# Kernel optimization log

Hardware: AMD Instinct MI355X
Metric: run time of the kernel (lower is better)

## Reference

```python
import jax, jax.numpy as jnp
import numpy as np

B, C, H, W, HEADS = 4, 192, 128, 128, 8
C2 = 2 * C
DN = ('NCHW', 'OIHW', 'NCHW')


def conv1x1(x, w, b):
    o = jax.lax.conv_general_dilated(x, w, (1, 1), 'VALID', dimension_numbers=DN)
    return o + b[None, :, None, None]


def gconv3(x, w, b):
    # grouped 3x3 conv: groups = C, channels = 2C -> 2 in / 2 out channels per group
    o = jax.lax.conv_general_dilated(x, w, (1, 1), 'SAME', dimension_numbers=DN,
                                     feature_group_count=C)
    return o + b[None, :, None, None]


def l2norm(t):
    # torch F.normalize(dim=-1, eps=1e-12)
    n = jnp.linalg.norm(t, axis=-1, keepdims=True)
    return t / jnp.maximum(n, 1e-12)


def setup_inputs() -> dict:
    key = jax.random.key(0)
    ks = jax.random.split(key, 16)
    s = 0.02
    inp = {
        'x': jax.random.normal(ks[0], (B, C, H, W), jnp.float32),
        'y': jax.random.normal(ks[1], (B, C, H, W), jnp.float32),
        'kv_w': jax.random.normal(ks[2], (C2, C, 1, 1), jnp.float32) * s,
        'kv_b': jax.random.normal(ks[3], (C2,), jnp.float32) * s,
        'kv_dw_w': jax.random.normal(ks[4], (C2, 2, 3, 3), jnp.float32) * s,
        'kv_dw_b': jax.random.normal(ks[5], (C2,), jnp.float32) * s,
        'q_w': jax.random.normal(ks[6], (C2, C, 1, 1), jnp.float32) * s,
        'q_b': jax.random.normal(ks[7], (C2,), jnp.float32) * s,
        'q_dw_w': jax.random.normal(ks[8], (C2, 2, 3, 3), jnp.float32) * s,
        'q_dw_b': jax.random.normal(ks[9], (C2,), jnp.float32) * s,
        'ky_w': jax.random.normal(ks[10], (C2, C, 1, 1), jnp.float32) * s,
        'ky_b': jax.random.normal(ks[11], (C2,), jnp.float32) * s,
        'ky_dw_w': jax.random.normal(ks[12], (C2, 2, 3, 3), jnp.float32) * s,
        'ky_dw_b': jax.random.normal(ks[13], (C2,), jnp.float32) * s,
        'temperature': jnp.ones((HEADS, 1, 1), jnp.float32),
        'gamma1': jnp.full((1,), 0.1, jnp.float32),
        'gamma2': jnp.full((1,), 0.1, jnp.float32),
    }
    return inp


def reference(x, y, kv_w, kv_b, kv_dw_w, kv_dw_b, q_w, q_b, q_dw_w, q_dw_b,
              ky_w, ky_b, ky_dw_w, ky_dw_b, temperature, gamma1, gamma2):
    b, c, h, w = x.shape
    ch = c // HEADS  # channels per head

    x_mid = x + y
    q = gconv3(conv1x1(x_mid, kv_w, kv_b), kv_dw_w, kv_dw_b)
    q1, q2 = jnp.split(q, 2, axis=1)
    kvx = gconv3(conv1x1(x, q_w, q_b), q_dw_w, q_dw_b)
    kx, vx = jnp.split(kvx, 2, axis=1)
    kvy = gconv3(conv1x1(y, ky_w, ky_b), ky_dw_w, ky_dw_b)
    ky_, vy = jnp.split(kvy, 2, axis=1)

    def to_heads(t):  # (b, head*ch, h, w) -> (b, head, ch, h*w)
        return t.reshape(b, HEADS, ch, h * w)

    q1, q2, kx, ky_, vx, vy = map(to_heads, (q1, q2, kx, ky_, vx, vy))
    q1, q2, kx, ky_ = map(l2norm, (q1, q2, kx, ky_))

    attn = (jnp.einsum('bhcn,bhdn->bhcd', q1, ky_) +
            jnp.einsum('bhcn,bhdn->bhcd', q2, kx)) * temperature[None]
    attn = jax.nn.softmax(attn, axis=-1)  # (b, head, c, c), tiny c

    out1 = jnp.einsum('bhcd,bhdn->bhcn', attn, vx)
    out2 = jnp.einsum('bhcd,bhdn->bhcn', attn, vy)
    out = gamma1[0] * out1 + gamma2[0] * out2
    return out.reshape(b, c, h, w)
```

## Files before the change

kernel.cpp:

```cpp
#include <hip/hip_runtime.h>
#include <hip/hip_bf16.h>
#include <stdint.h>

#define NUM_B 4
#define NUM_C 192
#define NUM_C2 384
#define NUM_H 128
#define NUM_W 128
#define NUM_N 16384
#define NHEADS 8
#define CHD 24

#define NKC 128
#define PSTRIDE 1280

typedef float f32x4_t __attribute__((ext_vector_type(4)));
typedef float f32x2_t __attribute__((ext_vector_type(2)));
typedef __bf16 bf16x8_t __attribute__((ext_vector_type(8)));
typedef unsigned short u16x8_t __attribute__((ext_vector_type(8)));

__device__ __forceinline__ float bf2f(unsigned short u){
  union { unsigned int i; float f; } v; v.i = ((unsigned int)u) << 16; return v.f;
}
__device__ __forceinline__ unsigned short f2bf(float f){
  union { float f; unsigned int i; } v; v.f = f;
  unsigned int x = v.i;
  x += 0x7fffu + ((x >> 16) & 1u);
  return (unsigned short)(x >> 16);
}
__device__ __forceinline__ unsigned short f2bf_n(float f){
  union { __bf16 h; unsigned short u; } cv; cv.h = (__bf16)f; return cv.u;
}

__global__ __launch_bounds__(256) void prepack_w3(
    const float* __restrict__ W0, const float* __restrict__ W1,
    const float* __restrict__ W2, unsigned short* __restrict__ out)
{
  int tid = blockIdx.x * 256 + threadIdx.x;
  if (tid >= 9216) return;
  const float* W = (blockIdx.y == 0) ? W0 : (blockIdx.y == 1) ? W1 : W2;
  unsigned short* o_ = out + (size_t)blockIdx.y * 73728;
  int c = tid & 3;
  int o = (tid >> 2) & 127;
  int s = (tid >> 9) % 6;
  int ot = tid / 3072;
  int sw = c ^ ((o >> 1) & 3);
  const float* src = W + (size_t)(ot * 128 + o) * NUM_C + s * 32 + sw * 8;
  f32x4_t f0 = *(const f32x4_t*)src;
  f32x4_t f1 = *(const f32x4_t*)(src + 4);
  u16x8_t pk;
  pk[0] = f2bf(f0[0]); pk[1] = f2bf(f0[1]); pk[2] = f2bf(f0[2]); pk[3] = f2bf(f0[3]);
  pk[4] = f2bf(f1[0]); pk[5] = f2bf(f1[1]); pk[6] = f2bf(f1[2]); pk[7] = f2bf(f1[3]);
  *(u16x8_t*)(o_ + (size_t)tid * 8) = pk;
}

__global__ __launch_bounds__(256) void prepack_in(
    const float* __restrict__ x, const float* __restrict__ y,
    unsigned short* __restrict__ xb, unsigned short* __restrict__ yb)
{
  const int t = threadIdx.x;
  const int nt = blockIdx.x, s = blockIdx.y, b = blockIdx.z;
  const float* px = x + (size_t)b * NUM_C * NUM_N + (size_t)s * 32 * NUM_N + nt * 128;
  const float* py = y + (size_t)b * NUM_C * NUM_N + (size_t)s * 32 * NUM_N + nt * 128;
  size_t obase = ((size_t)(b * 128 + nt) * 6 + s) * 4096;
  #pragma unroll
  for (int i = 0; i < 2; i++){
    int u = t + 256 * i;
    int n = u >> 2, slot = u & 3;
    int c = slot ^ ((n >> 1) & 3);
    const float* sx = px + (size_t)(c * 8) * NUM_N + n;
    const float* sy = py + (size_t)(c * 8) * NUM_N + n;
    u16x8_t ox, oy;
    #pragma unroll
    for (int kk = 0; kk < 8; kk++){
      ox[kk] = f2bf_n(sx[(size_t)kk * NUM_N]);
      oy[kk] = f2bf_n(sy[(size_t)kk * NUM_N]);
    }
    *(u16x8_t*)(xb + obase + (size_t)u * 8) = ox;
    *(u16x8_t*)(yb + obase + (size_t)u * 8) = oy;
  }
}

template<int ADD2>
__global__ __launch_bounds__(256, 4) void conv1x1_gemm(
    const unsigned short* __restrict__ Bpk0, const unsigned short* __restrict__ Bpk1,
    const unsigned short* __restrict__ Wpk, const float* __restrict__ bias,
    unsigned short* __restrict__ zout)
{
  __shared__ __align__(16) unsigned short As[2][4096];
  __shared__ __align__(16) unsigned short Bs[2][4096];
  const int d = blockIdx.x;
  const int xcd = d & 7;
  const int slot_ = d >> 3;
  const int ot = slot_ % 3;
  const int m_ = (slot_ / 3) * 8 + xcd;
  const int nt = m_ & 127;
  const int b = m_ >> 7;
  const int t = threadIdx.x;
  const int lane = t & 63;
  const int wv = t >> 6;
  const int wr = wv >> 1, wc = wv & 1;
  const int o0 = ot * 128;
  const int n0 = nt * 128;

  f32x4_t acc[4][4];
  const f32x4_t zz = {0.f, 0.f, 0.f, 0.f};
  #pragma unroll
  for (int m = 0; m < 4; m++)
    #pragma unroll
    for (int nf = 0; nf < 4; nf++) acc[m][nf] = zz;

  u16x8_t areg[2], breg[2], breg2[2];

  auto loadA = [&](int ks){
    const u16x8_t* gp = (const u16x8_t*)(Wpk + (size_t)(ot * 6 + ks) * 4096);
    areg[0] = gp[t];
    areg[1] = gp[t + 256];
  };
  auto loadB = [&](int ks){
    size_t off = ((size_t)(b * 128 + nt) * 6 + ks) * 4096;
    const u16x8_t* gp = (const u16x8_t*)(Bpk0 + off);
    breg[0] = gp[t];
    breg[1] = gp[t + 256];
    if (ADD2){
      const u16x8_t* gp2 = (const u16x8_t*)(Bpk1 + off);
      breg2[0] = gp2[t];
      breg2[1] = gp2[t + 256];
    }
  };
  auto writeA = [&](int buf){
    *(u16x8_t*)(&As[buf][(size_t)t * 8]) = areg[0];
    *(u16x8_t*)(&As[buf][(size_t)(t + 256) * 8]) = areg[1];
  };
  auto writeB = [&](int buf){
    if (!ADD2){
      *(u16x8_t*)(&Bs[buf][(size_t)t * 8]) = breg[0];
      *(u16x8_t*)(&Bs[buf][(size_t)(t + 256) * 8]) = breg[1];
    } else {
      #pragma unroll
      for (int i = 0; i < 2; i++){
        u16x8_t r;
        #pragma unroll
        for (int j = 0; j < 8; j++)
          r[j] = f2bf_n(bf2f(breg[i][j]) + bf2f(breg2[i][j]));
        *(u16x8_t*)(&Bs[buf][(size_t)(t + 256 * i) * 8]) = r;
      }
    }
  };

  auto compute = [&](int buf){
    const int rsel = lane & 15;
    const int g = lane >> 4;
    bf16x8_t af[4], bfr[4];
    #pragma unroll
    for (int m = 0; m < 4; m++){
      int r = wr * 64 + m * 16 + rsel;
      int sw = g ^ ((r >> 1) & 3);
      af[m] = *(const bf16x8_t*)(&As[buf][r * 32 + sw * 8]);
    }
    #pragma unroll
    for (int nf = 0; nf < 4; nf++){
      int r = wc * 64 + nf * 16 + rsel;
      int sw = g ^ ((r >> 1) & 3);
      bfr[nf] = *(const bf16x8_t*)(&Bs[buf][r * 32 + sw * 8]);
    }
    #pragma unroll
    for (int m = 0; m < 4; m++)
      #pragma unroll
      for (int nf = 0; nf < 4; nf++)
        acc[m][nf] = __builtin_amdgcn_mfma_f32_16x16x32_bf16(af[m], bfr[nf], acc[m][nf], 0, 0, 0);
  };

  loadA(0); loadB(0);
  writeA(0); writeB(0);
  __syncthreads();
  int buf = 0;
  #pragma unroll 1
  for (int ks = 0; ks < 6; ks++){
    if (ks < 5){
      loadA(ks + 1);
      loadB(ks + 1);
    }
    compute(buf);
    if (ks < 5){
      writeA(buf ^ 1);
      writeB(buf ^ 1);
      __syncthreads();
    }
    buf ^= 1;
  }

  const int colb = lane & 15;
  const int rsub = (lane >> 4) * 4;
  #pragma unroll
  for (int m = 0; m < 4; m++){
    #pragma unroll
    for (int nf = 0; nf < 4; nf++){
      int col = n0 + wc * 64 + nf * 16 + colb;
      #pragma unroll
      for (int r = 0; r < 4; r++){
        int o = o0 + wr * 64 + m * 16 + rsub + r;
        float v = acc[m][nf][r] + bias[o];
        zout[((size_t)b * NUM_C2 + o) * NUM_N + col] = f2bf_n(v);
      }
    }
  }
}

__global__ __launch_bounds__(256) void gconv3_dw(
    const unsigned short* __restrict__ z,
    const float* __restrict__ dww, const float* __restrict__ dwb,
    unsigned short* __restrict__ outq)
{
  const int t = threadIdx.x;
  const int wo = t & 15;
  const int hh = t >> 4;
  const int h = blockIdx.x * 16 + hh;
  const int g = blockIdx.y;
  const int b = blockIdx.z;

  float v[2][3][8];
  #pragma unroll
  for (int ic = 0; ic < 2; ic++){
    const unsigned short* src = z + ((size_t)b * NUM_C2 + 2 * g + ic) * NUM_N;
    #pragma unroll
    for (int dy = 0; dy < 3; dy++){
      int row = h + dy - 1;
      if (row >= 0 && row < NUM_H){
        u16x8_t raw = *(const u16x8_t*)(src + row * NUM_W + wo * 8);
        #pragma unroll
        for (int jj = 0; jj < 8; jj++) v[ic][dy][jj] = bf2f(raw[jj]);
      } else {
        #pragma unroll
        for (int jj = 0; jj < 8; jj++) v[ic][dy][jj] = 0.f;
      }
    }
  }
  float lft[2][3], rgt[2][3];
  #pragma unroll
  for (int ic = 0; ic < 2; ic++)
    #pragma unroll
    for (int dy = 0; dy < 3; dy++){
      float l = __shfl_up(v[ic][dy][7], 1u, 64);
      float r = __shfl_down(v[ic][dy][0], 1u, 64);
      lft[ic][dy] = (wo == 0)  ? 0.f : l;
      rgt[ic][dy] = (wo == 15) ? 0.f : r;
    }
  #pragma unroll
  for (int oc2 = 0; oc2 < 2; oc2++){
    const int oc = 2 * g + oc2;
    float wgt[2][9];
    #pragma unroll
    for (int ic = 0; ic < 2; ic++)
      #pragma unroll
      for (int k9 = 0; k9 < 9; k9++)
        wgt[ic][k9] = dww[(size_t)oc * 18 + ic * 9 + k9];
    float bia = dwb[oc];
    u16x8_t st;
    #pragma unroll
    for (int w8 = 0; w8 < 8; w8++){
      float s = bia;
      #pragma unroll
      for (int ic = 0; ic < 2; ic++)
        #pragma unroll
        for (int ky = 0; ky < 3; ky++)
          #pragma unroll
          for (int kx = 0; kx < 3; kx++){
            int wx = w8 + kx - 1;
            float xv = (wx < 0) ? lft[ic][ky] : ((wx > 7) ? rgt[ic][ky] : v[ic][ky][wx]);
            s += wgt[ic][ky * 3 + kx] * xv;
          }
      st[w8] = f2bf(s);
    }
    *(u16x8_t*)(outq + ((size_t)b * NUM_C2 + oc) * NUM_N + h * NUM_W + wo * 8) = st;
  }
}

__global__ __launch_bounds__(64) void dots_kernel(
    const unsigned short* __restrict__ qkv0, const unsigned short* __restrict__ qkv1,
    const unsigned short* __restrict__ qkv2, float* __restrict__ dpart)
{
  const int lane = threadIdx.x;
  const int kc = blockIdx.x;
  const int h = blockIdx.y;
  const int b = blockIdx.z;
  const unsigned short* q1 = qkv0 + ((size_t)b * NUM_C2 + h * CHD) * NUM_N;
  const unsigned short* q2 = qkv0 + ((size_t)b * NUM_C2 + NUM_C + h * CHD) * NUM_N;
  const unsigned short* kx = qkv1 + ((size_t)b * NUM_C2 + h * CHD) * NUM_N;
  const unsigned short* ky = qkv2 + ((size_t)b * NUM_C2 + h * CHD) * NUM_N;

  const f32x4_t zz = {0.f, 0.f, 0.f, 0.f};
  f32x4_t d1[2][2], d2[2][2], nrm[4][2];
  #pragma unroll
  for (int i = 0; i < 2; i++)
    #pragma unroll
    for (int j = 0; j < 2; j++){ d1[i][j] = zz; d2[i][j] = zz; }
  #pragma unroll
  for (int tn = 0; tn < 4; tn++){ nrm[tn][0] = zz; nrm[tn][1] = zz; }

  const int row = lane & 15;
  const int kl = (lane >> 4) * 8;
  const int r0 = row;
  const int r1 = (16 + row < CHD) ? (16 + row) : (CHD - 1);
  #pragma unroll
  for (int ks = 0; ks < 4; ks++){
    const size_t k0 = (size_t)kc * 128 + ks * 32 + kl;
    const size_t off0 = (size_t)r0 * NUM_N + k0;
    const size_t off1 = (size_t)r1 * NUM_N + k0;
    bf16x8_t fq1[2], fq2[2], fkx[2], fky[2];
    fq1[0] = *(const bf16x8_t*)(q1 + off0);  fq1[1] = *(const bf16x8_t*)(q1 + off1);
    fq2[0] = *(const bf16x8_t*)(q2 + off0);  fq2[1] = *(const bf16x8_t*)(q2 + off1);
    fkx[0] = *(const bf16x8_t*)(kx + off0);  fkx[1] = *(const bf16x8_t*)(kx + off1);
    fky[0] = *(const bf16x8_t*)(ky + off0);  fky[1] = *(const bf16x8_t*)(ky + off1);
    #pragma unroll
    for (int i = 0; i < 2; i++)
      #pragma unroll
      for (int j = 0; j < 2; j++){
        d1[i][j] = __builtin_amdgcn_mfma_f32_16x16x32_bf16(fq1[i], fky[j], d1[i][j], 0, 0, 0);
        d2[i][j] = __builtin_amdgcn_mfma_f32_16x16x32_bf16(fq2[i], fkx[j], d2[i][j], 0, 0, 0);
      }
    #pragma unroll
    for (int rg = 0; rg < 2; rg++){
      nrm[0][rg] = __builtin_amdgcn_mfma_f32_16x16x32_bf16(fq1[rg], fq1[rg], nrm[0][rg], 0, 0, 0);
      nrm[1][rg] = __builtin_amdgcn_mfma_f32_16x16x32_bf16(fq2[rg], fq2[rg], nrm[1][rg], 0, 0, 0);
      nrm[2][rg] = __builtin_amdgcn_mfma_f32_16x16x32_bf16(fkx[rg], fkx[rg], nrm[2][rg], 0, 0, 0);
      nrm[3][rg] = __builtin_amdgcn_mfma_f32_16x16x32_bf16(fky[rg], fky[rg], nrm[3][rg], 0, 0, 0);
    }
  }

  float* P = dpart + ((size_t)kc * (NUM_B * NHEADS) + (b * NHEADS + h)) * PSTRIDE;
  const int colb = lane & 15;
  const int rb = (lane >> 4) * 4;
  #pragma unroll
  for (int i = 0; i < 2; i++)
    #pragma unroll
    for (int j = 0; j < 2; j++){
      int cc = j * 16 + colb;
      if (cc < CHD){
        #pragma unroll
        for (int r = 0; r < 4; r++){
          int rr = i * 16 + rb + r;
          if (rr < CHD){
            P[rr * CHD + cc] = d1[i][j][r];
            P[576 + rr * CHD + cc] = d2[i][j][r];
          }
        }
      }
    }
  #pragma unroll
  for (int tn = 0; tn < 4; tn++)
    #pragma unroll
    for (int rg = 0; rg < 2; rg++){
      int cc = rg * 16 + colb;
      #pragma unroll
      for (int r = 0; r < 4; r++){
        int rr = rg * 16 + rb + r;
        if (rr == cc && rr < CHD) P[1152 + tn * CHD + rr] = nrm[tn][rg][r];
      }
    }
}

__global__ __launch_bounds__(256) void reduce_dots(
    const float* __restrict__ dpart,
    float* __restrict__ dots1, float* __restrict__ dots2, float* __restrict__ norms)
{
  const int slot = blockIdx.x * 256 + threadIdx.x;
  const int bh = blockIdx.y;
  if (slot >= 1248) return;
  float s = 0.f;
  #pragma unroll 4
  for (int kc = 0; kc < NKC; kc++)
    s += dpart[((size_t)kc * (NUM_B * NHEADS) + bh) * PSTRIDE + slot];
  if (slot < 576)        dots1[(size_t)bh * 576 + slot] = s;
  else if (slot < 1152)  dots2[(size_t)bh * 576 + (slot - 576)] = s;
  else                   norms[(size_t)bh * 96 + (slot - 1152)] = s;
}

__global__ __launch_bounds__(64) void softmax_kernel(
    const float* __restrict__ dots1, const float* __restrict__ dots2,
    const float* __restrict__ norms, const float* __restrict__ temp,
    float* __restrict__ attn)
{
  const int c = threadIdx.x;
  const int bh = blockIdx.x;
  if (c >= CHD) return;
  const int h = bh & 7;
  const float* D1 = dots1 + (size_t)bh * CHD * CHD;
  const float* D2 = dots2 + (size_t)bh * CHD * CHD;
  const float* NB = norms + (size_t)bh * 4 * CHD;
  float n1 = fmaxf(sqrtf(NB[0 * CHD + c]), 1e-12f);
  float n2 = fmaxf(sqrtf(NB[1 * CHD + c]), 1e-12f);
  float T = temp[h];
  float l[CHD];
  float m = -1e30f;
  #pragma unroll
  for (int d = 0; d < CHD; d++){
    float nx = fmaxf(sqrtf(NB[2 * CHD + d]), 1e-12f);
    float ny = fmaxf(sqrtf(NB[3 * CHD + d]), 1e-12f);
    float e = (D1[c * CHD + d] / (n1 * ny) + D2[c * CHD + d] / (n2 * nx)) * T;
    l[d] = e; m = fmaxf(m, e);
  }
  float s = 0.f;
  #pragma unroll
  for (int d = 0; d < CHD; d++){ float p = expf(l[d] - m); l[d] = p; s += p; }
  float inv = 1.f / s;
  float* A = attn + (size_t)bh * CHD * CHD + c * CHD;
  #pragma unroll
  for (int d = 0; d < CHD; d++) A[d] = l[d] * inv;
}

__global__ __launch_bounds__(256) void out_kernel(
    const unsigned short* __restrict__ qkv1, const unsigned short* __restrict__ qkv2,
    const float* __restrict__ attn,
    const float* __restrict__ g1, const float* __restrict__ g2,
    float* __restrict__ out)
{
  __shared__ float A[CHD * CHD];
  const int t = threadIdx.x;
  const int nc = blockIdx.x, hq = blockIdx.y, b = blockIdx.z;
  const float* Ag = attn + (size_t)(b * NHEADS + hq) * CHD * CHD;
  for (int i = t; i < CHD * CHD; i += 256) A[i] = Ag[i];
  __syncthreads();
  const int n = nc * 512 + t * 2;
  const unsigned short* vx = qkv1 + ((size_t)b * NUM_C2 + NUM_C + hq * CHD) * NUM_N + n;
  const unsigned short* vy = qkv2 + ((size_t)b * NUM_C2 + NUM_C + hq * CHD) * NUM_N + n;
  float vxa[CHD], vxb[CHD], vya[CHD], vyb[CHD];
  #pragma unroll
  for (int d = 0; d < CHD; d++){
    unsigned int rx = *(const unsigned int*)(vx + (size_t)d * NUM_N);
    unsigned int ry = *(const unsigned int*)(vy + (size_t)d * NUM_N);
    vxa[d] = bf2f((unsigned short)(rx & 0xffffu));
    vxb[d] = bf2f((unsigned short)(rx >> 16));
    vya[d] = bf2f((unsigned short)(ry & 0xffffu));
    vyb[d] = bf2f((unsigned short)(ry >> 16));
  }
  const float G1 = g1[0], G2 = g2[0];
  float* ob = out + ((size_t)b * NUM_C + hq * CHD) * NUM_N + n;
  #pragma unroll
  for (int cq = 0; cq < CHD; cq++){
    float ax = 0.f, bx = 0.f, ay = 0.f, by = 0.f;
    #pragma unroll
    for (int d = 0; d < CHD; d++){
      float a = A[cq * CHD + d];
      ax += a * vxa[d]; bx += a * vxb[d];
      ay += a * vya[d]; by += a * vyb[d];
    }
    f32x2_t st = {G1 * ax + G2 * ay, G1 * bx + G2 * by};
    *(f32x2_t*)(ob + (size_t)cq * NUM_N) = st;
  }
}

extern "C" void kernel_launch(void* const* d_in, const int* in_sizes, int n_in,
                              void* d_out, int out_size, void* d_ws, size_t ws_size,
                              hipStream_t stream)
{
  const float* x = (const float*)d_in[0];
  const float* y = (const float*)d_in[1];
  const float* conv_b[3] = {(const float*)d_in[3], (const float*)d_in[7], (const float*)d_in[11]};
  const float* dw_w[3]   = {(const float*)d_in[4], (const float*)d_in[8], (const float*)d_in[12]};
  const float* dw_b[3]   = {(const float*)d_in[5], (const float*)d_in[9], (const float*)d_in[13]};
  const float* conv_w[3] = {(const float*)d_in[2], (const float*)d_in[6], (const float*)d_in[10]};
  const float* temp = (const float*)d_in[14];
  const float* g1 = (const float*)d_in[15];
  const float* g2 = (const float*)d_in[16];
  float* out = (float*)d_out;

  char* ws = (char*)d_ws;
  unsigned short* xb   = (unsigned short*)ws;
  unsigned short* yb   = (unsigned short*)(ws + 25165824);
  unsigned short* qkv0 = (unsigned short*)ws;
  unsigned short* z    = (unsigned short*)(ws + 50331648);
  float* dpart         = (float*)(ws + 50331648);
  unsigned short* qkv1 = (unsigned short*)(ws + 100663296);
  unsigned short* qkv2 = (unsigned short*)(ws + 150994944);
  float* dots1 = (float*)(ws + 201326592);
  float* dots2 = dots1 + NUM_B * NHEADS * CHD * CHD;
  float* norms = dots2 + NUM_B * NHEADS * CHD * CHD;
  float* attn  = norms + NUM_B * NHEADS * 4 * CHD;
  unsigned short* Wpk = (unsigned short*)(attn + NUM_B * NHEADS * CHD * CHD);

  prepack_w3<<<dim3(36, 3), 256, 0, stream>>>(conv_w[0], conv_w[1], conv_w[2], Wpk);
  prepack_in<<<dim3(128, 6, NUM_B), 256, 0, stream>>>(x, y, xb, yb);

  dim3 gd(NUM_H / 16, NUM_C, NUM_B), bd(256);

  conv1x1_gemm<0><<<1536, 256, 0, stream>>>(xb, nullptr, Wpk + 1 * 73728, conv_b[1], z);
  gconv3_dw<<<gd, bd, 0, stream>>>(z, dw_w[1], dw_b[1], qkv1);
  conv1x1_gemm<0><<<1536, 256, 0, stream>>>(yb, nullptr, Wpk + 2 * 73728, conv_b[2], z);
  gconv3_dw<<<gd, bd, 0, stream>>>(z, dw_w[2], dw_b[2], qkv2);
  conv1x1_gemm<1><<<1536, 256, 0, stream>>>(xb, yb, Wpk + 0 * 73728, conv_b[0], z);
  gconv3_dw<<<gd, bd, 0, stream>>>(z, dw_w[0], dw_b[0], qkv0);

  dots_kernel<<<dim3(NKC, NHEADS, NUM_B), 64, 0, stream>>>(qkv0, qkv1, qkv2, dpart);
  reduce_dots<<<dim3(5, NUM_B * NHEADS), 256, 0, stream>>>(dpart, dots1, dots2, norms);
  softmax_kernel<<<dim3(NUM_B * NHEADS), 64, 0, stream>>>(dots1, dots2, norms, temp, attn);
  out_kernel<<<dim3(32, NHEADS, NUM_B), 256, 0, stream>>>(qkv1, qkv2, attn, g1, g2, out);
}
```

Baseline: 255.3 us.

## Stage GEMM epilogue through LDS for wide stores; vectorize input prepack loads

```diff
diff --git a/kernel.cpp b/kernel.cpp
--- a/kernel.cpp
+++ b/kernel.cpp
@@ -13,6 +13,7 @@
 
 #define NKC 128
 #define PSTRIDE 1280
+#define CPAD 140
 
 typedef float f32x4_t __attribute__((ext_vector_type(4)));
 typedef float f32x2_t __attribute__((ext_vector_type(2)));
@@ -59,25 +60,35 @@
     unsigned short* __restrict__ xb, unsigned short* __restrict__ yb)
 {
   const int t = threadIdx.x;
-  const int nt = blockIdx.x, s = blockIdx.y, b = blockIdx.z;
-  const float* px = x + (size_t)b * NUM_C * NUM_N + (size_t)s * 32 * NUM_N + nt * 128;
-  const float* py = y + (size_t)b * NUM_C * NUM_N + (size_t)s * 32 * NUM_N + nt * 128;
+  const int nt = blockIdx.x, ss = blockIdx.y, b = blockIdx.z;
+  const int sl = t >> 7;
+  const int tid = t & 127;
+  const int c = tid >> 5;
+  const int n4 = tid & 31;
+  const int s = ss * 2 + sl;
+
+  const float* pxb = x + (size_t)b * NUM_C * NUM_N + nt * 128 + n4 * 4;
+  const float* pyb = y + (size_t)b * NUM_C * NUM_N + nt * 128 + n4 * 4;
+  f32x4_t vx[8], vy[8];
+  #pragma unroll
+  for (int kk = 0; kk < 8; kk++){
+    size_t off = (size_t)(s * 32 + c * 8 + kk) * NUM_N;
+    vx[kk] = *(const f32x4_t*)(pxb + off);
+    vy[kk] = *(const f32x4_t*)(pyb + off);
+  }
   size_t obase = ((size_t)(b * 128 + nt) * 6 + s) * 4096;
   #pragma unroll
-  for (int i = 0; i < 2; i++){
-    int u = t + 256 * i;
-    int n = u >> 2, slot = u & 3;
-    int c = slot ^ ((n >> 1) & 3);
-    const float* sx = px + (size_t)(c * 8) * NUM_N + n;
-    const float* sy = py + (size_t)(c * 8) * NUM_N + n;
+  for (int j = 0; j < 4; j++){
+    int n = n4 * 4 + j;
+    int slot = c ^ ((n >> 1) & 3);
     u16x8_t ox, oy;
     #pragma unroll
     for (int kk = 0; kk < 8; kk++){
-      ox[kk] = f2bf_n(sx[(size_t)kk * NUM_N]);
-      oy[kk] = f2bf_n(sy[(size_t)kk * NUM_N]);
-    }
-    *(u16x8_t*)(xb + obase + (size_t)u * 8) = ox;
-    *(u16x8_t*)(yb + obase + (size_t)u * 8) = oy;
+      ox[kk] = f2bf_n(vx[kk][j]);
+      oy[kk] = f2bf_n(vy[kk][j]);
+    }
+    *(u16x8_t*)(xb + obase + (size_t)(n * 4 + slot) * 8) = ox;
+    *(u16x8_t*)(yb + obase + (size_t)(n * 4 + slot) * 8) = oy;
   }
 }
 
@@ -87,8 +98,9 @@
     const unsigned short* __restrict__ Wpk, const float* __restrict__ bias,
     unsigned short* __restrict__ zout)
 {
-  __shared__ __align__(16) unsigned short As[2][4096];
-  __shared__ __align__(16) unsigned short Bs[2][4096];
+  __shared__ __align__(16) unsigned short SH[128 * CPAD];
+  unsigned short* As0 = SH;
+  unsigned short* Bs0 = SH + 8192;
   const int d = blockIdx.x;
   const int xcd = d & 7;
   const int slot_ = d >> 3;
@@ -129,13 +141,13 @@
     }
   };
   auto writeA = [&](int buf){
-    *(u16x8_t*)(&As[buf][(size_t)t * 8]) = areg[0];
-    *(u16x8_t*)(&As[buf][(size_t)(t + 256) * 8]) = areg[1];
+    *(u16x8_t*)(As0 + buf * 4096 + (size_t)t * 8) = areg[0];
+    *(u16x8_t*)(As0 + buf * 4096 + (size_t)(t + 256) * 8) = areg[1];
   };
   auto writeB = [&](int buf){
     if (!ADD2){
-      *(u16x8_t*)(&Bs[buf][(size_t)t * 8]) = breg[0];
-      *(u16x8_t*)(&Bs[buf][(size_t)(t + 256) * 8]) = breg[1];
+      *(u16x8_t*)(Bs0 + buf * 4096 + (size_t)t * 8) = breg[0];
+      *(u16x8_t*)(Bs0 + buf * 4096 + (size_t)(t + 256) * 8) = breg[1];
     } else {
       #pragma unroll
       for (int i = 0; i < 2; i++){
@@ -143,7 +155,7 @@
         #pragma unroll
         for (int j = 0; j < 8; j++)
           r[j] = f2bf_n(bf2f(breg[i][j]) + bf2f(breg2[i][j]));
-        *(u16x8_t*)(&Bs[buf][(size_t)(t + 256 * i) * 8]) = r;
+        *(u16x8_t*)(Bs0 + buf * 4096 + (size_t)(t + 256 * i) * 8) = r;
       }
     }
   };
@@ -156,13 +168,13 @@
     for (int m = 0; m < 4; m++){
       int r = wr * 64 + m * 16 + rsel;
       int sw = g ^ ((r >> 1) & 3);
-      af[m] = *(const bf16x8_t*)(&As[buf][r * 32 + sw * 8]);
+      af[m] = *(const bf16x8_t*)(As0 + buf * 4096 + r * 32 + sw * 8);
     }
     #pragma unroll
     for (int nf = 0; nf < 4; nf++){
       int r = wc * 64 + nf * 16 + rsel;
       int sw = g ^ ((r >> 1) & 3);
-      bfr[nf] = *(const bf16x8_t*)(&Bs[buf][r * 32 + sw * 8]);
+      bfr[nf] = *(const bf16x8_t*)(Bs0 + buf * 4096 + r * 32 + sw * 8);
     }
     #pragma unroll
     for (int m = 0; m < 4; m++)
@@ -190,19 +202,35 @@
     buf ^= 1;
   }
 
-  const int colb = lane & 15;
-  const int rsub = (lane >> 4) * 4;
-  #pragma unroll
-  for (int m = 0; m < 4; m++){
-    #pragma unroll
-    for (int nf = 0; nf < 4; nf++){
-      int col = n0 + wc * 64 + nf * 16 + colb;
-      #pragma unroll
-      for (int r = 0; r < 4; r++){
-        int o = o0 + wr * 64 + m * 16 + rsub + r;
-        float v = acc[m][nf][r] + bias[o];
-        zout[((size_t)b * NUM_C2 + o) * NUM_N + col] = f2bf_n(v);
+  __syncthreads();
+  {
+    const int colb = lane & 15;
+    const int rsub = (lane >> 4) * 4;
+    #pragma unroll
+    for (int m = 0; m < 4; m++){
+      #pragma unroll
+      for (int nf = 0; nf < 4; nf++){
+        int col = wc * 64 + nf * 16 + colb;
+        #pragma unroll
+        for (int r = 0; r < 4; r++){
+          int row = wr * 64 + m * 16 + rsub + r;
+          SH[row * CPAD + col] = f2bf_n(acc[m][nf][r] + bias[o0 + row]);
+        }
       }
+    }
+  }
+  __syncthreads();
+  {
+    const int row = t >> 1;
+    const int half = t & 1;
+    const unsigned short* src = SH + row * CPAD + half * 64;
+    unsigned short* dst = zout + ((size_t)b * NUM_C2 + o0 + row) * NUM_N + n0 + half * 64;
+    #pragma unroll
+    for (int j = 0; j < 8; j++){
+      uint2 lo = *(const uint2*)(src + j * 8);
+      uint2 hi = *(const uint2*)(src + j * 8 + 4);
+      uint4 pk; pk.x = lo.x; pk.y = lo.y; pk.z = hi.x; pk.w = hi.y;
+      *(uint4*)(dst + j * 8) = pk;
     }
   }
 }
@@ -480,7 +508,7 @@
   unsigned short* Wpk = (unsigned short*)(attn + NUM_B * NHEADS * CHD * CHD);
 
   prepack_w3<<<dim3(36, 3), 256, 0, stream>>>(conv_w[0], conv_w[1], conv_w[2], Wpk);
-  prepack_in<<<dim3(128, 6, NUM_B), 256, 0, stream>>>(x, y, xb, yb);
+  prepack_in<<<dim3(128, 3, NUM_B), 256, 0, stream>>>(x, y, xb, yb);
 
   dim3 gd(NUM_H / 16, NUM_C, NUM_B), bd(256);
 
```

New measurement: 285.8 us. 11.9% more time.
